# Kernel optimization log

Hardware: AMD Instinct MI355X
Metric: run time of the kernel (lower is better)

Reference implementation:

```python
import jax, jax.numpy as jnp
import numpy as np

N = 49152   # nodes (1024 graphs * 48 teeth)
G = 1024    # graphs
E = 65536   # edges per relation
H, C, R = 8, 48, 3
FUSED = 384
NEG = 0.2   # RGATConv negative_slope default
EPS = 1e-5


def _ln_global(x, w, b):
    # PyG LayerNorm mode='graph' with batch=None: normalize over ALL elements
    x = x - jnp.mean(x)
    return x / (jnp.std(x) + EPS) * w + b


def _ln_graph(x, batch, w, b):
    # PyG LayerNorm mode='graph' with batch: per-graph mean/var over nodes+features
    f = x.shape[-1]
    cnt = jnp.maximum(jax.ops.segment_sum(jnp.ones((x.shape[0],), x.dtype), batch, num_segments=G), 1.0) * f
    mean = jax.ops.segment_sum(x, batch, num_segments=G).sum(-1) / cnt  # [G]
    xc = x - mean[batch][:, None]
    var = jax.ops.segment_sum(xc * xc, batch, num_segments=G).sum(-1) / cnt
    return xc / jnp.sqrt(var + EPS)[batch][:, None] * w + b


def _rgat(x, src, dst, etype, W, q, k, b):
    # RGATConv: per-relation transform, additive self-attention, across-relation segment softmax
    xt = jnp.einsum('nf,rfc->rnc', x, W)          # [R,N,H*C] transform once per relation
    oi = xt[etype, dst]                            # [E,H*C] destination (x_i) transformed
    oj = xt[etype, src]                            # [E,H*C] source (x_j) transformed
    alpha = jax.nn.leaky_relu(oi @ q + oj @ k, NEG)   # [E,H]
    m = jax.lax.stop_gradient(jax.ops.segment_max(alpha, dst, num_segments=N))
    a = jnp.exp(alpha - m[dst])
    s = jax.ops.segment_sum(a, dst, num_segments=N)
    a = a / (s[dst] + 1e-16)                       # segment softmax over in-edges per head
    msg = (a[:, :, None] * oj.reshape(-1, H, C)).reshape(-1, H * C)
    return jax.ops.segment_sum(msg, dst, num_segments=N) + b


def _enc(x, w, b, lw, lb):
    return _ln_global(jax.nn.relu(x @ w + b), lw, lb)


def _forward(floats, ei_o, ei_a, ei_s, batch):
    (x_visual, x_geom, x_prior, vis_w, vis_b, vis_lw, vis_lb, geom_w, geom_b, geom_lw, geom_lb,
     prior_w, prior_b, prior_lw, prior_lb, r1_w, r1_q, r1_k, r1_b, n1_w, n1_b,
     r2_w, r2_q, r2_k, r2_b, n2_w, n2_b, c_w1, c_b1, c_w2, c_b2) = floats
    ei = jnp.concatenate([ei_o, ei_a, ei_s], axis=1)
    etype = jnp.concatenate([jnp.zeros((ei_o.shape[1],), jnp.int32),
                             jnp.ones((ei_a.shape[1],), jnp.int32),
                             jnp.full((ei_s.shape[1],), 2, jnp.int32)])
    src, dst = ei[0], ei[1]
    h0 = jnp.concatenate([_enc(x_visual, vis_w, vis_b, vis_lw, vis_lb),
                          _enc(x_geom, geom_w, geom_b, geom_lw, geom_lb),
                          _enc(x_prior, prior_w, prior_b, prior_lw, prior_lb)], axis=-1)
    h1 = _ln_graph(h0 + jax.nn.elu(_rgat(h0, src, dst, etype, r1_w, r1_q, r1_k, r1_b)), batch, n1_w, n1_b)
    h2 = _ln_graph(h1 + jax.nn.elu(_rgat(h1, src, dst, etype, r2_w, r2_q, r2_k, r2_b)), batch, n2_w, n2_b)
    return jax.nn.relu(h2 @ c_w1 + c_b1) @ c_w2 + c_b2


def setup_inputs() -> dict:
    key = jax.random.key(0)
    ks = jax.random.split(key, 20)
    def rn(i, shape, s=0.05):
        return jax.random.normal(ks[i], shape, jnp.float32) * s
    return dict(
        x_visual=rn(0, (N, 1024), 1.0),
        x_geom=rn(1, (N, 6), 1.0),
        x_prior=rn(2, (N, 50), 1.0),
        vis_w=rn(3, (1024, 128)), vis_b=jnp.zeros((128,)), vis_lw=jnp.ones((128,)), vis_lb=jnp.zeros((128,)),
        geom_w=rn(4, (6, 128)), geom_b=jnp.zeros((128,)), geom_lw=jnp.ones((128,)), geom_lb=jnp.zeros((128,)),
        prior_w=rn(5, (50, 128)), prior_b=jnp.zeros((128,)), prior_lw=jnp.ones((128,)), prior_lb=jnp.zeros((128,)),
        r1_w=rn(6, (R, FUSED, H * C)), r1_q=rn(7, (H * C, H)), r1_k=rn(8, (H * C, H)), r1_b=jnp.zeros((H * C,)),
        n1_w=jnp.ones((FUSED,)), n1_b=jnp.zeros((FUSED,)),
        r2_w=rn(9, (R, FUSED, H * C)), r2_q=rn(10, (H * C, H)), r2_k=rn(11, (H * C, H)), r2_b=jnp.zeros((H * C,)),
        n2_w=jnp.ones((FUSED,)), n2_b=jnp.zeros((FUSED,)),
        c_w1=rn(12, (FUSED, 128)), c_b1=jnp.zeros((128,)), c_w2=rn(13, (128, 49)), c_b2=jnp.zeros((49,)),
        edge_index_overlap=jax.random.randint(ks[14], (2, E), 0, N),
        edge_index_arch=jax.random.randint(ks[15], (2, E), 0, N),
        edge_index_spatial=jax.random.randint(ks[16], (2, E), 0, N),
        batch=jnp.sort(jax.random.randint(ks[17], (N,), 0, G)),
    )


def reference(x_visual, x_geom, x_prior, vis_w, vis_b, vis_lw, vis_lb, geom_w, geom_b, geom_lw, geom_lb, prior_w, prior_b, prior_lw, prior_lb, r1_w, r1_q, r1_k, r1_b, n1_w, n1_b, r2_w, r2_q, r2_k, r2_b, n2_w, n2_b, c_w1, c_b1, c_w2, c_b2, edge_index_overlap, edge_index_arch, edge_index_spatial, batch):
    floats = (x_visual, x_geom, x_prior, vis_w, vis_b, vis_lw, vis_lb, geom_w, geom_b, geom_lw, geom_lb,
              prior_w, prior_b, prior_lw, prior_lb, r1_w, r1_q, r1_k, r1_b, n1_w, n1_b,
              r2_w, r2_q, r2_k, r2_b, n2_w, n2_b, c_w1, c_b1, c_w2, c_b2)
    return _forward(floats, edge_index_overlap, edge_index_arch, edge_index_spatial, batch)
```

## Files before the change

kernel.cpp:

```cpp
#include <hip/hip_runtime.h>
#include <hip/hip_bf16.h>

#define NN 49152
#define GG 1024
#define EE 65536
#define ETOT 196608
#define FF 384
#define NEG_SLOPE 0.2f

typedef __attribute__((ext_vector_type(8))) short bf16x8;
typedef __attribute__((ext_vector_type(4))) float f32x4;

__device__ __forceinline__ float wave_sum(float v) {
#pragma unroll
    for (int m = 32; m; m >>= 1) v += __shfl_xor(v, m);
    return v;
}
__device__ __forceinline__ unsigned short f2bf(float f) {
    __hip_bfloat16 b = __float2bfloat16(f);
    return *reinterpret_cast<unsigned short*>(&b);
}
__device__ __forceinline__ float bflo(unsigned u) { return __uint_as_float(u << 16); }
__device__ __forceinline__ float bfhi(unsigned u) { return __uint_as_float(u & 0xffff0000u); }
__device__ __forceinline__ unsigned pk2(float lo, float hi) {
    return ((unsigned)f2bf(hi) << 16) | (unsigned)f2bf(lo);
}

__device__ __forceinline__ void gload_lds16(const void* g, void* l) {
    __builtin_amdgcn_global_load_lds(
        (const __attribute__((address_space(1))) unsigned int*)g,
        (__attribute__((address_space(3))) unsigned int*)l, 16, 0, 0);
}

__device__ __forceinline__ int swz(int row, int c16) {
    return row * 64 + ((c16 ^ ((row >> 1) & 3)) << 4);
}

template <int ACT, bool ABF, bool OBF>
__global__ __launch_bounds__(256) void gemm_mfma(
    const void* __restrict__ Ag, int K,
    const unsigned short* __restrict__ Btg,
    const float* __restrict__ bias,
    void* __restrict__ Cg, int ldc,
    size_t bzs, size_t czs)
{
    __shared__ __align__(16) char As[8192];
    __shared__ __align__(16) char Bs[8192];
    const unsigned short* Bt = Btg + (size_t)blockIdx.z * bzs;
    int t = threadIdx.x;
    int bm = blockIdx.x << 7, bn = blockIdx.y << 7;
    int lane = t & 63, wid = t >> 6, wr = wid >> 1, wc = wid & 1;
    f32x4 acc[4][4] = {};
    int ktn = K >> 5;
    for (int kt = 0; kt < ktn; ++kt) {
        int k0 = kt << 5;
#pragma unroll
        for (int ii = 0; ii < 2; ++ii) {
            int id = t + (ii << 8);
            int row = id >> 2, c = id & 3;
            int csrc = c ^ ((row >> 1) & 3);
            size_t ldsoff = (size_t)((wid << 10) + (ii << 12));
            if (ABF) {
                const unsigned short* srcA = (const unsigned short*)Ag + (size_t)(bm + row) * K + k0 + csrc * 8;
                gload_lds16(srcA, As + ldsoff);
            } else {
                const float* srcA = (const float*)Ag + (size_t)(bm + row) * K + k0 + c * 8;
                float4 a0 = *(const float4*)srcA;
                float4 a1 = *(const float4*)(srcA + 4);
                union { unsigned short u[8]; int4 v; } P;
                P.u[0] = f2bf(a0.x); P.u[1] = f2bf(a0.y); P.u[2] = f2bf(a0.z); P.u[3] = f2bf(a0.w);
                P.u[4] = f2bf(a1.x); P.u[5] = f2bf(a1.y); P.u[6] = f2bf(a1.z); P.u[7] = f2bf(a1.w);
                *(int4*)(As + swz(row, c)) = P.v;
            }
            const unsigned short* srcB = Bt + (size_t)(bn + row) * K + k0 + csrc * 8;
            gload_lds16(srcB, Bs + ldsoff);
        }
        __syncthreads();
        int c16 = lane >> 4;
        bf16x8 af[4], bfr[4];
#pragma unroll
        for (int m = 0; m < 4; ++m)
            af[m] = *(const bf16x8*)(As + swz((wr << 6) + (m << 4) + (lane & 15), c16));
#pragma unroll
        for (int n = 0; n < 4; ++n)
            bfr[n] = *(const bf16x8*)(Bs + swz((wc << 6) + (n << 4) + (lane & 15), c16));
#pragma unroll
        for (int m = 0; m < 4; ++m)
#pragma unroll
            for (int n = 0; n < 4; ++n)
                acc[m][n] = __builtin_amdgcn_mfma_f32_16x16x32_bf16(af[m], bfr[n], acc[m][n], 0, 0, 0);
        __syncthreads();
    }
#pragma unroll
    for (int m = 0; m < 4; ++m) {
#pragma unroll
        for (int n = 0; n < 4; ++n) {
            int row0 = bm + (wr << 6) + (m << 4) + ((lane >> 4) << 2);
            int col = bn + (wc << 6) + (n << 4) + (lane & 15);
            float bv = bias ? bias[col] : 0.f;
#pragma unroll
            for (int j = 0; j < 4; ++j) {
                float v = acc[m][n][j] + bv;
                if (ACT == 1) v = fmaxf(v, 0.f);
                if (OBF) {
                    unsigned short* C = (unsigned short*)Cg + (size_t)blockIdx.z * czs;
                    C[(size_t)(row0 + j) * ldc + col] = f2bf(v);
                } else {
                    float* C = (float*)Cg + (size_t)blockIdx.z * czs;
                    C[(size_t)(row0 + j) * ldc + col] = v;
                }
            }
        }
    }
}

template <int ACT, bool OBF>
__global__ __launch_bounds__(256) void gemm_k(
    const float* __restrict__ A, int K,
    const float* __restrict__ W, int Jw,
    const float* __restrict__ bias,
    void* __restrict__ Cg, int ldc, int jmax)
{
    __shared__ float Ash[16][64];
    __shared__ float Bsh[16][68];
    int tid = threadIdx.x;
    int bj = blockIdx.x << 6;
    int bm = blockIdx.y << 6;
    int tx = tid & 15, ty = tid >> 4;
    float acc[4][4] = {};
    int ktn = (K + 15) >> 4;
    int ar = tid >> 2;
    int aks = (tid & 3) << 2;
    int wk = tid >> 4;
    int wjs = (tid & 15) << 2;
    for (int kt = 0; kt < ktn; ++kt) {
        int k0 = kt << 4;
        const float* Ap = A + (size_t)(bm + ar) * K + k0 + aks;
#pragma unroll
        for (int i = 0; i < 4; ++i) {
            int k = k0 + aks + i;
            Ash[aks + i][ar] = (k < K) ? Ap[i] : 0.f;
        }
        const float* Wp = W + (size_t)(k0 + wk) * Jw + bj + wjs;
        bool kok = (k0 + wk) < K;
#pragma unroll
        for (int i = 0; i < 4; ++i) {
            int j = bj + wjs + i;
            Bsh[wk][wjs + i] = (kok && j < jmax) ? Wp[i] : 0.f;
        }
        __syncthreads();
#pragma unroll
        for (int kk = 0; kk < 16; ++kk) {
            const float4 av = *reinterpret_cast<const float4*>(&Ash[kk][ty << 2]);
            const float4 bv = *reinterpret_cast<const float4*>(&Bsh[kk][tx << 2]);
            float aa[4] = {av.x, av.y, av.z, av.w};
            float bb[4] = {bv.x, bv.y, bv.z, bv.w};
#pragma unroll
            for (int i = 0; i < 4; ++i)
#pragma unroll
                for (int j = 0; j < 4; ++j)
                    acc[i][j] = fmaf(aa[i], bb[j], acc[i][j]);
        }
        __syncthreads();
    }
#pragma unroll
    for (int i = 0; i < 4; ++i) {
        int row = bm + (ty << 2) + i;
#pragma unroll
        for (int j = 0; j < 4; ++j) {
            int col = bj + (tx << 2) + j;
            if (col < jmax) {
                float v = acc[i][j];
                if (bias) v += bias[col];
                if (ACT == 1) v = fmaxf(v, 0.f);
                if (OBF) ((unsigned short*)Cg)[(size_t)row * ldc + col] = f2bf(v);
                else     ((float*)Cg)[(size_t)row * ldc + col] = v;
            }
        }
    }
}

__global__ void transpose_bf(const float* __restrict__ W, unsigned short* __restrict__ Wt,
                             int K, int N, int total) {
    int i = blockIdx.x * 256 + threadIdx.x;
    if (i >= total) return;
    int kn = K * N;
    int z = i / kn, rem = i - z * kn;
    int k = rem / N, n = rem - k * N;
    Wt[(size_t)z * kn + (size_t)n * K + k] = f2bf(W[i]);
}

__global__ __launch_bounds__(256) void wqk_prep(
    const float* __restrict__ rw, const float* __restrict__ q, const float* __restrict__ k,
    unsigned short* __restrict__ wqkt)
{
    __shared__ float qsT[16 * 384];
    int t = threadIdx.x;
    int r = blockIdx.x, ftile = blockIdx.y;
    for (int idx = t; idx < 384 * 16; idx += 256) {
        int c = idx >> 4, j = idx & 15;
        qsT[j * 384 + c] = (j < 8) ? q[c * 8 + j] : k[c * 8 + j - 8];
    }
    __syncthreads();
    int j = t & 15, fi = t >> 4;
    const float4* q4 = (const float4*)(qsT + j * 384);
#pragma unroll
    for (int rr = 0; rr < 4; ++rr) {
        int f = ftile * 64 + fi * 4 + rr;
        const float4* a4 = (const float4*)(rw + (size_t)r * FF * FF + (size_t)f * FF);
        float dot = 0.f;
        for (int c4 = 0; c4 < 96; ++c4) {
            float4 a = a4[c4], b = q4[c4];
            dot += a.x * b.x + a.y * b.y + a.z * b.z + a.w * b.w;
        }
        wqkt[(size_t)(r * 16 + j) * FF + f] = f2bf(dot);
    }
}

__global__ void csr_count(const int* __restrict__ eo, const int* __restrict__ ea,
                          const int* __restrict__ es, int* __restrict__ deg) {
    int e = blockIdx.x * 256 + threadIdx.x;
    if (e >= ETOT) return;
    int et = e >> 16, le = e & 65535;
    const int* ei = et == 0 ? eo : (et == 1 ? ea : es);
    atomicAdd(&deg[ei[EE + le]], 1);
}
__global__ void csr_alloc(const int* __restrict__ deg, int* __restrict__ counter,
                          int* __restrict__ rps) {
    int n = blockIdx.x * 256 + threadIdx.x;
    int lane = threadIdx.x & 63;
    int d = (n < NN) ? deg[n] : 0;
    int x = d;
#pragma unroll
    for (int off = 1; off < 64; off <<= 1) {
        int y = __shfl_up(x, off);
        if (lane >= off) x += y;
    }
    int total = __shfl(x, 63);
    int base = 0;
    if (lane == 63) base = atomicAdd(counter, total);
    base = __shfl(base, 63);
    if (n < NN) rps[n] = base + x - d;
}
__global__ void csr_fill(const int* __restrict__ eo, const int* __restrict__ ea,
                         const int* __restrict__ es, const int* __restrict__ rps,
                         int* __restrict__ fill, int* __restrict__ elist) {
    int e = blockIdx.x * 256 + threadIdx.x;
    if (e >= ETOT) return;
    int et = e >> 16, le = e & 65535;
    const int* ei = et == 0 ? eo : (et == 1 ? ea : es);
    int src = ei[le], dst = ei[EE + le];
    int pos = rps[dst] + atomicAdd(&fill[dst], 1);
    elist[pos] = (et << 16) | src;
}

__global__ void count_nodes(const int* __restrict__ batch, float* __restrict__ gcnt) {
    int n = blockIdx.x * 256 + threadIdx.x;
    if (n < NN) atomicAdd(&gcnt[batch[n]], 1.f);
}

#define ERB 512
__global__ __launch_bounds__(256) void enc_reduce_stage1(const unsigned short* __restrict__ hb, float* __restrict__ pbuf) {
    __shared__ float part[4][6];
    float a1 = 0.f, a2 = 0.f, b1 = 0.f, b2 = 0.f, c1 = 0.f, c2 = 0.f;
    const uint4* h8 = (const uint4*)hb;
    int total8 = NN * FF / 8;
    for (int i = blockIdx.x * 256 + threadIdx.x; i < total8; i += ERB * 256) {
        uint4 v = h8[i];
        float e0 = bflo(v.x), e1 = bfhi(v.x), e2 = bflo(v.y), e3 = bfhi(v.y);
        float e4 = bflo(v.z), e5 = bfhi(v.z), e6 = bflo(v.w), e7 = bfhi(v.w);
        float s1 = e0 + e1 + e2 + e3 + e4 + e5 + e6 + e7;
        float s2 = e0*e0 + e1*e1 + e2*e2 + e3*e3 + e4*e4 + e5*e5 + e6*e6 + e7*e7;
        int enc = (i % 48) >> 4;
        if (enc == 0)      { a1 += s1; a2 += s2; }
        else if (enc == 1) { b1 += s1; b2 += s2; }
        else               { c1 += s1; c2 += s2; }
    }
    a1 = wave_sum(a1); a2 = wave_sum(a2);
    b1 = wave_sum(b1); b2 = wave_sum(b2);
    c1 = wave_sum(c1); c2 = wave_sum(c2);
    int w = threadIdx.x >> 6;
    if ((threadIdx.x & 63) == 0) {
        part[w][0] = a1; part[w][1] = a2; part[w][2] = b1;
        part[w][3] = b2; part[w][4] = c1; part[w][5] = c2;
    }
    __syncthreads();
    if (threadIdx.x < 6) {
        float s = part[0][threadIdx.x] + part[1][threadIdx.x] + part[2][threadIdx.x] + part[3][threadIdx.x];
        pbuf[blockIdx.x * 6 + threadIdx.x] = s;
    }
}

__global__ void enc_reduce_stage2(const float* __restrict__ pbuf, float* __restrict__ est) {
    int lane = threadIdx.x;
    float s[6] = {};
    for (int b = lane; b < ERB; b += 64)
#pragma unroll
        for (int j = 0; j < 6; ++j) s[j] += pbuf[b * 6 + j];
#pragma unroll
    for (int j = 0; j < 6; ++j) {
        float v = wave_sum(s[j]);
        if (lane == 0) est[j] = v;
    }
    __syncthreads();
    if (lane < 3) {
        float cnt = (float)NN * 128.f;
        float mean = est[2 * lane] / cnt;
        float var = est[2 * lane + 1] / cnt - mean * mean;
        var = fmaxf(var, 0.f);
        est[6 + 2 * lane] = mean;
        est[7 + 2 * lane] = 1.f / (sqrtf(var) + 1e-5f);
    }
}

__global__ __launch_bounds__(256) void enc_apply(
    unsigned short* __restrict__ hb, const float* __restrict__ est,
    const float* __restrict__ lw0, const float* __restrict__ lb0,
    const float* __restrict__ lw1, const float* __restrict__ lb1,
    const float* __restrict__ lw2, const float* __restrict__ lb2)
{
    long gt = (long)blockIdx.x * 256 + threadIdx.x;
    if (gt >= (long)NN * FF) return;
    int f = (int)(gt % FF);
    int enc = f >> 7, j = f & 127;
    const float* lw = enc == 0 ? lw0 : (enc == 1 ? lw1 : lw2);
    const float* lb = enc == 0 ? lb0 : (enc == 1 ? lb1 : lb2);
    float mean = est[6 + 2 * enc], sc = est[7 + 2 * enc];
    float v = (bflo((unsigned)hb[gt]) - mean) * sc * lw[j] + lb[j];
    hb[gt] = f2bf(v);
}

__global__ __launch_bounds__(256) void qk48_mfma(
    const unsigned short* __restrict__ hb,
    const unsigned short* __restrict__ wqkt,
    float* __restrict__ qkbuf)
{
    __shared__ __align__(16) unsigned short wlds[48 * 392];
    int t = threadIdx.x;
    for (int idx = t; idx < 48 * 192; idx += 256) {
        int row = idx / 192, dw = idx - row * 192;
        *((unsigned*)(wlds + row * 392) + dw) = ((const unsigned*)wqkt)[row * 192 + dw];
    }
    __syncthreads();
    int lane = t & 63, wid = t >> 6;
    int col = lane & 15, kq = lane >> 4;
    int tile = blockIdx.x * 4 + wid;
    const unsigned short* arow = hb + (size_t)(tile * 16 + col) * FF + kq * 8;
    f32x4 acc0 = {}, acc1 = {}, acc2 = {};
#pragma unroll
    for (int kt = 0; kt < 12; ++kt) {
        bf16x8 af = *(const bf16x8*)(arow + kt * 32);
        bf16x8 b0 = *(const bf16x8*)(wlds + (0 * 16 + col) * 392 + kt * 32 + kq * 8);
        bf16x8 b1 = *(const bf16x8*)(wlds + (1 * 16 + col) * 392 + kt * 32 + kq * 8);
        bf16x8 b2 = *(const bf16x8*)(wlds + (2 * 16 + col) * 392 + kt * 32 + kq * 8);
        acc0 = __builtin_amdgcn_mfma_f32_16x16x32_bf16(af, b0, acc0, 0, 0, 0);
        acc1 = __builtin_amdgcn_mfma_f32_16x16x32_bf16(af, b1, acc1, 0, 0, 0);
        acc2 = __builtin_amdgcn_mfma_f32_16x16x32_bf16(af, b2, acc2, 0, 0, 0);
    }
    int row0 = kq << 2;
#pragma unroll
    for (int j = 0; j < 4; ++j) {
        size_t node = (size_t)tile * 16 + row0 + j;
        qkbuf[node * 48 + 0 + col]  = acc0[j];
        qkbuf[node * 48 + 16 + col] = acc1[j];
        qkbuf[node * 48 + 32 + col] = acc2[j];
    }
}

__global__ __launch_bounds__(256) void gather_fused(
    const int* __restrict__ rps, const int* __restrict__ deg, const int* __restrict__ elist,
    const float* __restrict__ qkbuf, const unsigned short* __restrict__ xt,
    const unsigned short* __restrict__ hbin, const float* __restrict__ rb, const int* __restrict__ batch,
    float* __restrict__ gs1, float* __restrict__ gs2, unsigned short* __restrict__ ybuf)
{
    int node = blockIdx.x * 4 + (threadIdx.x >> 6);
    int lane = threadIdx.x & 63;
    int d = deg[node], rp = rps[node];
    int head = lane >> 3;
    float qd0 = qkbuf[(size_t)node * 48 + 0 + head];
    float qd1 = qkbuf[(size_t)node * 48 + 16 + head];
    float qd2 = qkbuf[(size_t)node * 48 + 32 + head];
    float s = 0.f;
    float acc0 = 0.f, acc1 = 0.f, acc2 = 0.f, acc3 = 0.f, acc4 = 0.f, acc5 = 0.f;
    for (int e = 0; e < d; ++e) {
        int packed = elist[rp + e];
        int et = packed >> 16, src = packed & 0xFFFF;
        const unsigned* xr = (const unsigned*)(xt + ((size_t)et * NN + src) * FF) + lane * 3;
        unsigned u0 = xr[0], u1 = xr[1], u2 = xr[2];
        float qd = et == 0 ? qd0 : (et == 1 ? qd1 : qd2);
        float a = qd + qkbuf[(size_t)src * 48 + et * 16 + 8 + head];
        a = a >= 0.f ? a : NEG_SLOPE * a;
        float pw = __expf(a);
        s += pw;
        acc0 = fmaf(pw, bflo(u0), acc0); acc1 = fmaf(pw, bfhi(u0), acc1);
        acc2 = fmaf(pw, bflo(u1), acc2); acc3 = fmaf(pw, bfhi(u1), acc3);
        acc4 = fmaf(pw, bflo(u2), acc4); acc5 = fmaf(pw, bfhi(u2), acc5);
    }
    float inv = 1.f / (s + 1e-16f);
    const unsigned* hr = (const unsigned*)(hbin + (size_t)node * FF) + lane * 3;
    unsigned h0u = hr[0], h1u = hr[1], h2u = hr[2];
    float hv[6] = {bflo(h0u), bfhi(h0u), bflo(h1u), bfhi(h1u), bflo(h2u), bfhi(h2u)};
    float av[6] = {acc0, acc1, acc2, acc3, acc4, acc5};
    int f0 = lane * 6;
    float s1 = 0.f, s2 = 0.f;
    float yv[6];
#pragma unroll
    for (int i = 0; i < 6; ++i) {
        float mv = av[i] * inv + rb[f0 + i];
        float e = mv > 0.f ? mv : (__expf(mv) - 1.f);
        float y = hv[i] + e;
        yv[i] = y;
        s1 += y; s2 += y * y;
    }
    unsigned* yrow = (unsigned*)(ybuf + (size_t)node * FF) + lane * 3;
    yrow[0] = pk2(yv[0], yv[1]);
    yrow[1] = pk2(yv[2], yv[3]);
    yrow[2] = pk2(yv[4], yv[5]);
    s1 = wave_sum(s1);
    s2 = wave_sum(s2);
    if (lane == 0) {
        int g = batch[node];
        atomicAdd(&gs1[g], s1);
        atomicAdd(&gs2[g], s2);
    }
}

__global__ __launch_bounds__(256) void ln_apply(
    const unsigned short* __restrict__ y, const int* __restrict__ batch,
    const float* __restrict__ gcnt, const float* __restrict__ gs1, const float* __restrict__ gs2,
    const float* __restrict__ w, const float* __restrict__ b,
    unsigned short* __restrict__ hbOut)
{
    long gt = (long)blockIdx.x * 256 + threadIdx.x;
    int n = (int)(gt >> 6);
    if (n >= NN) return;
    int lane = (int)(gt & 63);
    int f0 = lane * 6;
    int g = batch[n];
    float cnt = fmaxf(gcnt[g], 1.f) * (float)FF;
    float mean = gs1[g] / cnt;
    float var = fmaxf(gs2[g] / cnt - mean * mean, 0.f);
    float rs = 1.f / sqrtf(var + 1e-5f);
    const unsigned* yr = (const unsigned*)(y + (size_t)n * FF) + lane * 3;
    unsigned u0 = yr[0], u1 = yr[1], u2 = yr[2];
    float yv[6] = {bflo(u0), bfhi(u0), bflo(u1), bfhi(u1), bflo(u2), bfhi(u2)};
    float ov[6];
#pragma unroll
    for (int i = 0; i < 6; ++i)
        ov[i] = (yv[i] - mean) * rs * w[f0 + i] + b[f0 + i];
    unsigned* orow = (unsigned*)(hbOut + (size_t)n * FF) + lane * 3;
    orow[0] = pk2(ov[0], ov[1]);
    orow[1] = pk2(ov[2], ov[3]);
    orow[2] = pk2(ov[4], ov[5]);
}

static void rgat_layer(hipStream_t stream,
    const unsigned short* hbIn,
    const float* rw, const float* rq, const float* rk, const float* rb,
    const float* lnw, const float* lnb,
    const int* rps, const int* deg, const int* elist, const int* batch,
    unsigned short* wt, unsigned short* xt, unsigned short* wqkt, float* qkbuf,
    float* gsbuf, const float* gcnt,
    unsigned short* ybuf, unsigned short* hbOut)
{
    hipMemsetAsync(gsbuf, 0, 2 * GG * 4, stream);
    int tt = 3 * FF * FF;
    transpose_bf<<<(tt + 255) / 256, 256, 0, stream>>>(rw, wt, FF, FF, tt);
    wqk_prep<<<dim3(3, 6), 256, 0, stream>>>(rw, rq, rk, wqkt);
    gemm_mfma<0, true, true><<<dim3(384, 3, 3), 256, 0, stream>>>(
        hbIn, FF, wt, nullptr, xt, FF, (size_t)FF * FF, (size_t)NN * FF);
    qk48_mfma<<<NN / 64, 256, 0, stream>>>(hbIn, wqkt, qkbuf);
    gather_fused<<<NN / 4, 256, 0, stream>>>(rps, deg, elist, qkbuf, xt, hbIn, rb, batch,
                                             gsbuf, gsbuf + GG, ybuf);
    ln_apply<<<NN / 4, 256, 0, stream>>>(ybuf, batch, gcnt, gsbuf, gsbuf + GG, lnw, lnb, hbOut);
}

extern "C" void kernel_launch(void* const* d_in, const int* in_sizes, int n_in,
                              void* d_out, int out_size, void* d_ws, size_t ws_size,
                              hipStream_t stream)
{
    const float* x_visual = (const float*)d_in[0];
    const float* x_geom   = (const float*)d_in[1];
    const float* x_prior  = (const float*)d_in[2];
    const float* vis_w  = (const float*)d_in[3];
    const float* vis_b  = (const float*)d_in[4];
    const float* vis_lw = (const float*)d_in[5];
    const float* vis_lb = (const float*)d_in[6];
    const float* geom_w  = (const float*)d_in[7];
    const float* geom_b  = (const float*)d_in[8];
    const float* geom_lw = (const float*)d_in[9];
    const float* geom_lb = (const float*)d_in[10];
    const float* prior_w  = (const float*)d_in[11];
    const float* prior_b  = (const float*)d_in[12];
    const float* prior_lw = (const float*)d_in[13];
    const float* prior_lb = (const float*)d_in[14];
    const float* r1_w = (const float*)d_in[15];
    const float* r1_q = (const float*)d_in[16];
    const float* r1_k = (const float*)d_in[17];
    const float* r1_b = (const float*)d_in[18];
    const float* n1_w = (const float*)d_in[19];
    const float* n1_b = (const float*)d_in[20];
    const float* r2_w = (const float*)d_in[21];
    const float* r2_q = (const float*)d_in[22];
    const float* r2_k = (const float*)d_in[23];
    const float* r2_b = (const float*)d_in[24];
    const float* n2_w = (const float*)d_in[25];
    const float* n2_b = (const float*)d_in[26];
    const float* c_w1 = (const float*)d_in[27];
    const float* c_b1 = (const float*)d_in[28];
    const float* c_w2 = (const float*)d_in[29];
    const float* c_b2 = (const float*)d_in[30];
    const int* ei_o  = (const int*)d_in[31];
    const int* ei_a  = (const int*)d_in[32];
    const int* ei_s  = (const int*)d_in[33];
    const int* batch = (const int*)d_in[34];
    float* out = (float*)d_out;

    char* p = (char*)d_ws;
    auto alloc = [&](size_t bytes) { char* r = p; p += (bytes + 255) & ~(size_t)255; return r; };
    unsigned short* hbA = (unsigned short*)alloc((size_t)NN * FF * 2);
    unsigned short* hbB = (unsigned short*)alloc((size_t)NN * FF * 2);
    unsigned short* ybuf = (unsigned short*)alloc((size_t)NN * FF * 2);
    unsigned short* xt = (unsigned short*)alloc((size_t)3 * NN * FF * 2);
    unsigned short* wt = (unsigned short*)alloc((size_t)3 * FF * FF * 2);
    float* qkbuf = (float*)alloc((size_t)NN * 48 * 4);
    unsigned short* wqkt = (unsigned short*)alloc((size_t)48 * FF * 2);
    float* t128 = (float*)alloc((size_t)NN * 128 * 4);
    int* degfill = (int*)alloc((size_t)2 * NN * 4);
    int* deg = degfill;
    int* fill = degfill + NN;
    int* rps = (int*)alloc(NN * 4);
    int* elist = (int*)alloc(ETOT * 4);
    int* counter = (int*)alloc(256);
    float* gsbuf = (float*)alloc((size_t)2 * GG * 4);
    float* gcnt = (float*)alloc(GG * 4);
    float* est = (float*)alloc(64);
    float* pbuf = (float*)alloc(ERB * 6 * 4);

    hipMemsetAsync(degfill, 0, (size_t)2 * NN * 4, stream);
    hipMemsetAsync(counter, 0, 4, stream);
    csr_count<<<ETOT / 256, 256, 0, stream>>>(ei_o, ei_a, ei_s, deg);
    csr_alloc<<<NN / 256, 256, 0, stream>>>(deg, counter, rps);
    csr_fill<<<ETOT / 256, 256, 0, stream>>>(ei_o, ei_a, ei_s, rps, fill, elist);

    hipMemsetAsync(gcnt, 0, GG * 4, stream);
    count_nodes<<<NN / 256, 256, 0, stream>>>(batch, gcnt);

    transpose_bf<<<(1024 * 128 + 255) / 256, 256, 0, stream>>>(vis_w, wt, 1024, 128, 1024 * 128);
    gemm_mfma<1, false, true><<<dim3(384, 1, 1), 256, 0, stream>>>(
        x_visual, 1024, wt, vis_b, hbA, FF, 0, 0);
    gemm_k<1, true><<<dim3(2, 768, 1), 256, 0, stream>>>(x_geom, 6, geom_w, 128, geom_b, hbA + 128, FF, 128);
    gemm_k<1, true><<<dim3(2, 768, 1), 256, 0, stream>>>(x_prior, 50, prior_w, 128, prior_b, hbA + 256, FF, 128);
    enc_reduce_stage1<<<ERB, 256, 0, stream>>>(hbA, pbuf);
    enc_reduce_stage2<<<1, 64, 0, stream>>>(pbuf, est);
    enc_apply<<<(int)((size_t)NN * FF / 256), 256, 0, stream>>>(
        hbA, est, vis_lw, vis_lb, geom_lw, geom_lb, prior_lw, prior_lb);

    rgat_layer(stream, hbA, r1_w, r1_q, r1_k, r1_b, n1_w, n1_b,
               rps, deg, elist, batch, wt, xt, wqkt, qkbuf, gsbuf, gcnt, ybuf, hbB);
    rgat_layer(stream, hbB, r2_w, r2_q, r2_k, r2_b, n2_w, n2_b,
               rps, deg, elist, batch, wt, xt, wqkt, qkbuf, gsbuf, gcnt, ybuf, hbA);

    transpose_bf<<<(FF * 128 + 255) / 256, 256, 0, stream>>>(c_w1, wt, FF, 128, FF * 128);
    gemm_mfma<1, true, false><<<dim3(384, 1, 1), 256, 0, stream>>>(
        hbA, FF, wt, c_b1, t128, 128, 0, 0);
    gemm_k<0, false><<<dim3(1, 768, 1), 256, 0, stream>>>(t128, 128, c_w2, 49, c_b2, out, 49, 49);
}
```

Measured before the change: 748.2 us.

## Batch weight prep and memsets upfront, fold node counting, cooperatively load edge lists

Moves the weight transposes and q/k weight folding for both RGAT layers and the classifier into a few combined launches at the start. Zero-initialised buffers now share one contiguous region cleared by a single memset, and per-graph node counting is folded into csr_alloc. In the gather kernel, each wave loads up to 64 edge entries at once and broadcasts them with shuffles instead of every lane reading each entry. The intent is fewer launches and memsets and less redundant edge-list traffic, at the cost of extra workspace for per-layer weight copies.

```diff
diff --git a/kernel.cpp b/kernel.cpp
--- a/kernel.cpp
+++ b/kernel.cpp
@@ -190,13 +190,29 @@
     Wt[(size_t)z * kn + (size_t)n * K + k] = f2bf(W[i]);
 }
 
-__global__ __launch_bounds__(256) void wqk_prep(
-    const float* __restrict__ rw, const float* __restrict__ q, const float* __restrict__ k,
-    unsigned short* __restrict__ wqkt)
+__global__ void transpose2_bf(const float* __restrict__ W1, const float* __restrict__ W2,
+                              unsigned short* __restrict__ Wt1, unsigned short* __restrict__ Wt2) {
+    int i = blockIdx.x * 256 + threadIdx.x;
+    if (i >= 6 * FF * FF) return;
+    int z = i / (FF * FF), rem = i - z * (FF * FF);
+    int k = rem / FF, n = rem - k * FF;
+    const float* W = (z < 3) ? W1 + (size_t)z * FF * FF : W2 + (size_t)(z - 3) * FF * FF;
+    unsigned short* Wt = (z < 3) ? Wt1 + (size_t)z * FF * FF : Wt2 + (size_t)(z - 3) * FF * FF;
+    Wt[(size_t)n * FF + k] = f2bf(W[(size_t)k * FF + n]);
+}
+
+__global__ __launch_bounds__(256) void wqk_prep2(
+    const float* __restrict__ rw1, const float* __restrict__ q1, const float* __restrict__ k1,
+    const float* __restrict__ rw2, const float* __restrict__ q2, const float* __restrict__ k2,
+    unsigned short* __restrict__ wqkt1, unsigned short* __restrict__ wqkt2)
 {
     __shared__ float qsT[16 * 384];
     int t = threadIdx.x;
-    int r = blockIdx.x, ftile = blockIdx.y;
+    int r = blockIdx.x, ftile = blockIdx.y, layer = blockIdx.z;
+    const float* rw = layer ? rw2 : rw1;
+    const float* q = layer ? q2 : q1;
+    const float* k = layer ? k2 : k1;
+    unsigned short* wqkt = layer ? wqkt2 : wqkt1;
     for (int idx = t; idx < 384 * 16; idx += 256) {
         int c = idx >> 4, j = idx & 15;
         qsT[j * 384 + c] = (j < 8) ? q[c * 8 + j] : k[c * 8 + j - 8];
@@ -226,7 +242,8 @@
     atomicAdd(&deg[ei[EE + le]], 1);
 }
 __global__ void csr_alloc(const int* __restrict__ deg, int* __restrict__ counter,
-                          int* __restrict__ rps) {
+                          int* __restrict__ rps, const int* __restrict__ batch,
+                          float* __restrict__ gcnt) {
     int n = blockIdx.x * 256 + threadIdx.x;
     int lane = threadIdx.x & 63;
     int d = (n < NN) ? deg[n] : 0;
@@ -240,7 +257,10 @@
     int base = 0;
     if (lane == 63) base = atomicAdd(counter, total);
     base = __shfl(base, 63);
-    if (n < NN) rps[n] = base + x - d;
+    if (n < NN) {
+        rps[n] = base + x - d;
+        atomicAdd(&gcnt[batch[n]], 1.f);
+    }
 }
 __global__ void csr_fill(const int* __restrict__ eo, const int* __restrict__ ea,
                          const int* __restrict__ es, const int* __restrict__ rps,
@@ -252,11 +272,6 @@
     int src = ei[le], dst = ei[EE + le];
     int pos = rps[dst] + atomicAdd(&fill[dst], 1);
     elist[pos] = (et << 16) | src;
-}
-
-__global__ void count_nodes(const int* __restrict__ batch, float* __restrict__ gcnt) {
-    int n = blockIdx.x * 256 + threadIdx.x;
-    if (n < NN) atomicAdd(&gcnt[batch[n]], 1.f);
 }
 
 #define ERB 512
@@ -380,25 +395,29 @@
     float qd0 = qkbuf[(size_t)node * 48 + 0 + head];
     float qd1 = qkbuf[(size_t)node * 48 + 16 + head];
     float qd2 = qkbuf[(size_t)node * 48 + 32 + head];
+    const unsigned* hr = (const unsigned*)(hbin + (size_t)node * FF) + lane * 3;
+    unsigned h0u = hr[0], h1u = hr[1], h2u = hr[2];
     float s = 0.f;
     float acc0 = 0.f, acc1 = 0.f, acc2 = 0.f, acc3 = 0.f, acc4 = 0.f, acc5 = 0.f;
-    for (int e = 0; e < d; ++e) {
-        int packed = elist[rp + e];
-        int et = packed >> 16, src = packed & 0xFFFF;
-        const unsigned* xr = (const unsigned*)(xt + ((size_t)et * NN + src) * FF) + lane * 3;
-        unsigned u0 = xr[0], u1 = xr[1], u2 = xr[2];
-        float qd = et == 0 ? qd0 : (et == 1 ? qd1 : qd2);
-        float a = qd + qkbuf[(size_t)src * 48 + et * 16 + 8 + head];
-        a = a >= 0.f ? a : NEG_SLOPE * a;
-        float pw = __expf(a);
-        s += pw;
-        acc0 = fmaf(pw, bflo(u0), acc0); acc1 = fmaf(pw, bfhi(u0), acc1);
-        acc2 = fmaf(pw, bflo(u1), acc2); acc3 = fmaf(pw, bfhi(u1), acc3);
-        acc4 = fmaf(pw, bflo(u2), acc4); acc5 = fmaf(pw, bfhi(u2), acc5);
+    for (int base = 0; base < d; base += 64) {
+        int myp = (base + lane < d) ? elist[rp + base + lane] : 0;
+        int lim = d - base; if (lim > 64) lim = 64;
+        for (int e = 0; e < lim; ++e) {
+            int packed = __shfl(myp, e);
+            int et = packed >> 16, src = packed & 0xFFFF;
+            const unsigned* xr = (const unsigned*)(xt + ((size_t)et * NN + src) * FF) + lane * 3;
+            unsigned u0 = xr[0], u1 = xr[1], u2 = xr[2];
+            float qd = et == 0 ? qd0 : (et == 1 ? qd1 : qd2);
+            float a = qd + qkbuf[(size_t)src * 48 + et * 16 + 8 + head];
+            a = a >= 0.f ? a : NEG_SLOPE * a;
+            float pw = __expf(a);
+            s += pw;
+            acc0 = fmaf(pw, bflo(u0), acc0); acc1 = fmaf(pw, bfhi(u0), acc1);
+            acc2 = fmaf(pw, bflo(u1), acc2); acc3 = fmaf(pw, bfhi(u1), acc3);
+            acc4 = fmaf(pw, bflo(u2), acc4); acc5 = fmaf(pw, bfhi(u2), acc5);
+        }
     }
     float inv = 1.f / (s + 1e-16f);
-    const unsigned* hr = (const unsigned*)(hbin + (size_t)node * FF) + lane * 3;
-    unsigned h0u = hr[0], h1u = hr[1], h2u = hr[2];
     float hv[6] = {bflo(h0u), bfhi(h0u), bflo(h1u), bfhi(h1u), bflo(h2u), bfhi(h2u)};
     float av[6] = {acc0, acc1, acc2, acc3, acc4, acc5};
     int f0 = lane * 6;
@@ -456,23 +475,18 @@
 
 static void rgat_layer(hipStream_t stream,
     const unsigned short* hbIn,
-    const float* rw, const float* rq, const float* rk, const float* rb,
-    const float* lnw, const float* lnb,
+    const float* rb, const float* lnw, const float* lnb,
     const int* rps, const int* deg, const int* elist, const int* batch,
-    unsigned short* wt, unsigned short* xt, unsigned short* wqkt, float* qkbuf,
-    float* gsbuf, const float* gcnt,
+    const unsigned short* wt, unsigned short* xt, const unsigned short* wqkt, float* qkbuf,
+    float* gs, const float* gcnt,
     unsigned short* ybuf, unsigned short* hbOut)
 {
-    hipMemsetAsync(gsbuf, 0, 2 * GG * 4, stream);
-    int tt = 3 * FF * FF;
-    transpose_bf<<<(tt + 255) / 256, 256, 0, stream>>>(rw, wt, FF, FF, tt);
-    wqk_prep<<<dim3(3, 6), 256, 0, stream>>>(rw, rq, rk, wqkt);
     gemm_mfma<0, true, true><<<dim3(384, 3, 3), 256, 0, stream>>>(
         hbIn, FF, wt, nullptr, xt, FF, (size_t)FF * FF, (size_t)NN * FF);
     qk48_mfma<<<NN / 64, 256, 0, stream>>>(hbIn, wqkt, qkbuf);
     gather_fused<<<NN / 4, 256, 0, stream>>>(rps, deg, elist, qkbuf, xt, hbIn, rb, batch,
-                                             gsbuf, gsbuf + GG, ybuf);
-    ln_apply<<<NN / 4, 256, 0, stream>>>(ybuf, batch, gcnt, gsbuf, gsbuf + GG, lnw, lnb, hbOut);
+                                             gs, gs + GG, ybuf);
+    ln_apply<<<NN / 4, 256, 0, stream>>>(ybuf, batch, gcnt, gs, gs + GG, lnw, lnb, hbOut);
 }
 
 extern "C" void kernel_launch(void* const* d_in, const int* in_sizes, int n_in,
@@ -522,33 +536,37 @@
     unsigned short* hbB = (unsigned short*)alloc((size_t)NN * FF * 2);
     unsigned short* ybuf = (unsigned short*)alloc((size_t)NN * FF * 2);
     unsigned short* xt = (unsigned short*)alloc((size_t)3 * NN * FF * 2);
-    unsigned short* wt = (unsigned short*)alloc((size_t)3 * FF * FF * 2);
+    unsigned short* wt1 = (unsigned short*)alloc((size_t)3 * FF * FF * 2);
+    unsigned short* wt2 = (unsigned short*)alloc((size_t)3 * FF * FF * 2);
+    unsigned short* wtv = (unsigned short*)alloc((size_t)1024 * 128 * 2);
+    unsigned short* wtc = (unsigned short*)alloc((size_t)FF * 128 * 2);
     float* qkbuf = (float*)alloc((size_t)NN * 48 * 4);
-    unsigned short* wqkt = (unsigned short*)alloc((size_t)48 * FF * 2);
+    unsigned short* wqkt1 = (unsigned short*)alloc((size_t)48 * FF * 2);
+    unsigned short* wqkt2 = (unsigned short*)alloc((size_t)48 * FF * 2);
     float* t128 = (float*)alloc((size_t)NN * 128 * 4);
-    int* degfill = (int*)alloc((size_t)2 * NN * 4);
-    int* deg = degfill;
-    int* fill = degfill + NN;
     int* rps = (int*)alloc(NN * 4);
     int* elist = (int*)alloc(ETOT * 4);
-    int* counter = (int*)alloc(256);
-    float* gsbuf = (float*)alloc((size_t)2 * GG * 4);
-    float* gcnt = (float*)alloc(GG * 4);
     float* est = (float*)alloc(64);
     float* pbuf = (float*)alloc(ERB * 6 * 4);
-
-    hipMemsetAsync(degfill, 0, (size_t)2 * NN * 4, stream);
-    hipMemsetAsync(counter, 0, 4, stream);
+    char* z0 = alloc((size_t)2 * NN * 4 + 256 + (size_t)4 * GG * 4 + GG * 4);
+    int* deg = (int*)z0;
+    int* fill = deg + NN;
+    int* counter = (int*)(z0 + (size_t)2 * NN * 4);
+    float* gs = (float*)(z0 + (size_t)2 * NN * 4 + 256);
+    float* gcnt = gs + 4 * GG;
+    hipMemsetAsync(z0, 0, (size_t)2 * NN * 4 + 256 + (size_t)4 * GG * 4 + GG * 4, stream);
+
     csr_count<<<ETOT / 256, 256, 0, stream>>>(ei_o, ei_a, ei_s, deg);
-    csr_alloc<<<NN / 256, 256, 0, stream>>>(deg, counter, rps);
+    csr_alloc<<<NN / 256, 256, 0, stream>>>(deg, counter, rps, batch, gcnt);
     csr_fill<<<ETOT / 256, 256, 0, stream>>>(ei_o, ei_a, ei_s, rps, fill, elist);
 
-    hipMemsetAsync(gcnt, 0, GG * 4, stream);
-    count_nodes<<<NN / 256, 256, 0, stream>>>(batch, gcnt);
-
-    transpose_bf<<<(1024 * 128 + 255) / 256, 256, 0, stream>>>(vis_w, wt, 1024, 128, 1024 * 128);
+    transpose2_bf<<<(6 * FF * FF + 255) / 256, 256, 0, stream>>>(r1_w, r2_w, wt1, wt2);
+    wqk_prep2<<<dim3(3, 6, 2), 256, 0, stream>>>(r1_w, r1_q, r1_k, r2_w, r2_q, r2_k, wqkt1, wqkt2);
+    transpose_bf<<<(1024 * 128 + 255) / 256, 256, 0, stream>>>(vis_w, wtv, 1024, 128, 1024 * 128);
+    transpose_bf<<<(FF * 128 + 255) / 256, 256, 0, stream>>>(c_w1, wtc, FF, 128, FF * 128);
+
     gemm_mfma<1, false, true><<<dim3(384, 1, 1), 256, 0, stream>>>(
-        x_visual, 1024, wt, vis_b, hbA, FF, 0, 0);
+        x_visual, 1024, wtv, vis_b, hbA, FF, 0, 0);
     gemm_k<1, true><<<dim3(2, 768, 1), 256, 0, stream>>>(x_geom, 6, geom_w, 128, geom_b, hbA + 128, FF, 128);
     gemm_k<1, true><<<dim3(2, 768, 1), 256, 0, stream>>>(x_prior, 50, prior_w, 128, prior_b, hbA + 256, FF, 128);
     enc_reduce_stage1<<<ERB, 256, 0, stream>>>(hbA, pbuf);
@@ -556,13 +574,12 @@
     enc_apply<<<(int)((size_t)NN * FF / 256), 256, 0, stream>>>(
         hbA, est, vis_lw, vis_lb, geom_lw, geom_lb, prior_lw, prior_lb);
 
-    rgat_layer(stream, hbA, r1_w, r1_q, r1_k, r1_b, n1_w, n1_b,
-               rps, deg, elist, batch, wt, xt, wqkt, qkbuf, gsbuf, gcnt, ybuf, hbB);
-    rgat_layer(stream, hbB, r2_w, r2_q, r2_k, r2_b, n2_w, n2_b,
-               rps, deg, elist, batch, wt, xt, wqkt, qkbuf, gsbuf, gcnt, ybuf, hbA);
-
-    transpose_bf<<<(FF * 128 + 255) / 256, 256, 0, stream>>>(c_w1, wt, FF, 128, FF * 128);
+    rgat_layer(stream, hbA, r1_b, n1_w, n1_b, rps, deg, elist, batch,
+               wt1, xt, wqkt1, qkbuf, gs, gcnt, ybuf, hbB);
+    rgat_layer(stream, hbB, r2_b, n2_w, n2_b, rps, deg, elist, batch,
+               wt2, xt, wqkt2, qkbuf, gs + 2 * GG, gcnt, ybuf, hbA);
+
     gemm_mfma<1, true, false><<<dim3(384, 1, 1), 256, 0, stream>>>(
-        hbA, FF, wt, c_b1, t128, 128, 0, 0);
+        hbA, FF, wtc, c_b1, t128, 128, 0, 0);
     gemm_k<0, false><<<dim3(1, 768, 1), 256, 0, stream>>>(t128, 128, c_w2, 49, c_b2, out, 49, 49);
 }
```

Result: faster. 700.6 us (-6.4%).
